# Performance work log

Measured on AMD Instinct MI355X. Metric: run time of the kernel, lower is better.

Reference implementation:

```python
import jax, jax.numpy as jnp
import numpy as np

N = 100000
E = 1600000
DIM_IN, DIM_H, DIM_OUT = 48, 48, 48


def gcn_conv(x, edge_index, W, b):
    # PyG GCNConv: add self-loops, symmetric normalization D^-1/2 (A+I) D^-1/2, linear first.
    n = x.shape[0]
    loop = jnp.arange(n, dtype=edge_index.dtype)
    row = jnp.concatenate([edge_index[0], loop])  # sources
    col = jnp.concatenate([edge_index[1], loop])  # targets
    deg = jax.ops.segment_sum(jnp.ones_like(col, dtype=x.dtype), col, num_segments=n)
    dinv = jnp.where(deg > 0, jax.lax.rsqrt(jnp.maximum(deg, 1e-12)), 0.0)
    norm = dinv[row] * dinv[col]  # [E+N]
    h = x @ W  # [N, out]
    msg = h[row] * norm[:, None]  # gather + scale, [E+N, out]
    out = jax.ops.segment_sum(msg, col, num_segments=n)  # scatter-add
    return out + b


def setup_inputs() -> dict:
    key = jax.random.key(0)
    ks = jax.random.split(key, 8)
    x = jax.random.normal(ks[0], (N, DIM_IN), dtype=jnp.float32)
    edge_index = jax.random.randint(ks[1], (2, E), 0, N, dtype=jnp.int64)
    s1 = 1.0 / np.sqrt(DIM_IN)
    s2 = 1.0 / np.sqrt(DIM_H)
    s3 = 1.0 / np.sqrt(DIM_OUT)
    W1 = jax.random.uniform(ks[2], (DIM_IN, DIM_H), jnp.float32, -s1, s1)
    b1 = jnp.zeros((DIM_H,), jnp.float32)
    W2 = jax.random.uniform(ks[3], (DIM_H, DIM_OUT), jnp.float32, -s2, s2)
    b2 = jnp.zeros((DIM_OUT,), jnp.float32)
    Wlin = jax.random.uniform(ks[4], (DIM_OUT, 2), jnp.float32, -s3, s3)
    blin = jax.random.uniform(ks[5], (2,), jnp.float32, -s3, s3)
    return {"x": x, "edge_index": edge_index, "W1": W1, "b1": b1, "W2": W2, "b2": b2, "Wlin": Wlin, "blin": blin}


def reference(x, edge_index, W1, b1, W2, b2, Wlin, blin):
    h = gcn_conv(x, edge_index, W1, b1)
    h = jax.nn.leaky_relu(h, negative_slope=0.01)
    h = gcn_conv(h, edge_index, W2, b2)
    # global_add_pool with all-zero batch ids -> sum over all nodes, [1, DIM_OUT]
    g = jnp.sum(h, axis=0, keepdims=True)
    # dropout is identity in eval mode
    return g @ Wlin + blin  # [1, 2]
```

## Files before the change

### kernel.cpp

```cpp
#include <hip/hip_runtime.h>
#include <hip/hip_bf16.h>
#include <hip/hip_fp8.h>

#define DIM 48
#define HS8 64
#define BKN 128
#define NB1MAX 800
#define NBLK 512
#define BCAPE 3072
#define GNPB 64
#define GTPN 3

typedef float v2f __attribute__((ext_vector_type(2)));

__device__ inline unsigned pack_fp8x4(float a, float b, float c, float d) {
#if __has_builtin(__builtin_amdgcn_cvt_pk_fp8_f32)
    int w = __builtin_amdgcn_cvt_pk_fp8_f32(a, b, 0, false);
    w = __builtin_amdgcn_cvt_pk_fp8_f32(c, d, w, true);
    return (unsigned)w;
#else
    __hip_fp8_e4m3 qa(a), qb(b), qc(c), qd(d);
    return (unsigned)qa.__x | ((unsigned)qb.__x << 8) |
           ((unsigned)qc.__x << 16) | ((unsigned)qd.__x << 24);
#endif
}

__device__ inline void acc_fp8x4(unsigned w, float* acc) {
#if __has_builtin(__builtin_amdgcn_cvt_pk_f32_fp8)
    v2f lo = __builtin_amdgcn_cvt_pk_f32_fp8((int)w, false);
    v2f hi = __builtin_amdgcn_cvt_pk_f32_fp8((int)w, true);
    acc[0] += lo[0]; acc[1] += lo[1]; acc[2] += hi[0]; acc[3] += hi[1];
#else
    __hip_fp8_e4m3 q0, q1, q2, q3;
    q0.__x = (unsigned char)(w & 0xff);
    q1.__x = (unsigned char)((w >> 8) & 0xff);
    q2.__x = (unsigned char)((w >> 16) & 0xff);
    q3.__x = (unsigned char)(w >> 24);
    acc[0] += (float)q0; acc[1] += (float)q1;
    acc[2] += (float)q2; acc[3] += (float)q3;
#endif
}

__global__ void k_bh(const int* __restrict__ col, int* __restrict__ bh, int E, int nb1) {
    __shared__ int h[NB1MAX];
    for (int i = threadIdx.x; i < nb1; i += blockDim.x) h[i] = 0;
    __syncthreads();
    int chunk = (E + NBLK - 1) / NBLK;
    int lo = blockIdx.x * chunk, hi = min(lo + chunk, E);
    for (int e = lo + threadIdx.x; e < hi; e += blockDim.x)
        atomicAdd(&h[col[e] >> 7], 1);
    __syncthreads();
    int* r = bh + (size_t)blockIdx.x * nb1;
    for (int i = threadIdx.x; i < nb1; i += blockDim.x) r[i] = h[i];
}

__global__ void k_colscan(int* __restrict__ bh, int* __restrict__ coltot, int nb1) {
    __shared__ int sm[NBLK];
    int b = blockIdx.x, t = threadIdx.x;
    sm[t] = bh[(size_t)t * nb1 + b];
    __syncthreads();
    int val = sm[t];
    for (int off = 1; off < NBLK; off <<= 1) {
        int v = (t >= off) ? sm[t - off] : 0;
        __syncthreads();
        sm[t] += v;
        __syncthreads();
    }
    bh[(size_t)t * nb1 + b] = sm[t] - val;
    if (t == NBLK - 1) coltot[b] = sm[t];
}

__global__ void k_scan1(const int* __restrict__ coltot, int* __restrict__ bstart,
                        float* __restrict__ g, int* __restrict__ nodeoff,
                        int nb1, int N, int E) {
    __shared__ int sm[1024];
    int t = threadIdx.x;
    sm[t] = (t < nb1) ? coltot[t] : 0;
    __syncthreads();
    for (int off = 1; off < 1024; off <<= 1) {
        int v = (t >= off) ? sm[t - off] : 0;
        __syncthreads();
        sm[t] += v;
        __syncthreads();
    }
    if (t < nb1) bstart[t] = (t == 0) ? 0 : sm[t - 1];
    if (t == 0) { bstart[nb1] = E; nodeoff[N] = E; }
    if (t < 64) g[t] = 0.0f;
}

__global__ void k_part2(const int* __restrict__ row, const int* __restrict__ col,
                        const int* __restrict__ bh, const int* __restrict__ bstart,
                        unsigned* __restrict__ part, int E, int nb1) {
    __shared__ int base[NB1MAX];
    __shared__ int lcur[NB1MAX];
    int blk = blockIdx.x, t = threadIdx.x;
    const int* bhr = bh + (size_t)blk * nb1;
    for (int i = t; i < nb1; i += blockDim.x) { base[i] = bstart[i] + bhr[i]; lcur[i] = 0; }
    __syncthreads();
    int chunk = (E + NBLK - 1) / NBLK;
    int lo = blk * chunk, hi = min(lo + chunk, E);
    for (int e = lo + t; e < hi; e += blockDim.x) {
        int c = col[e], r = row[e];
        int b = c >> 7;
        int s = atomicAdd(&lcur[b], 1);
        part[base[b] + s] = ((unsigned)(c & 127) << 24) | (unsigned)r;
    }
}

__global__ void k_sort(const unsigned* __restrict__ part, const int* __restrict__ bstart,
                       int* __restrict__ nodeoff, float* __restrict__ dinv,
                       int* __restrict__ srcs, int N, int nb1) {
    __shared__ int cnt[BKN];
    __shared__ int cur[BKN];
    __shared__ int sc[256];
    __shared__ int outb[BCAPE];
    int b = blockIdx.x, t = threadIdx.x;
    int nlo = b * BKN;
    int elo = bstart[b], ehi = bstart[b + 1];
    int nE = ehi - elo;
    if (t < BKN) cnt[t] = 0;
    __syncthreads();
    for (int e = elo + t; e < ehi; e += blockDim.x)
        atomicAdd(&cnt[part[e] >> 24], 1);
    __syncthreads();
    int v = (t < BKN) ? cnt[t] : 0;
    sc[t] = v;
    __syncthreads();
    for (int off = 1; off < 256; off <<= 1) {
        int u = (t >= off) ? sc[t - off] : 0;
        __syncthreads();
        sc[t] += u;
        __syncthreads();
    }
    int ex = (t == 0) ? 0 : sc[t - 1];
    if (t < BKN && nlo + t < N) {
        nodeoff[nlo + t] = elo + ex;
        dinv[nlo + t] = 1.0f / sqrtf((float)(v + 1));
        cur[t] = ex;
    }
    __syncthreads();
    if (nE <= BCAPE) {
        for (int e = elo + t; e < ehi; e += blockDim.x) {
            unsigned p = part[e];
            int s = atomicAdd(&cur[p >> 24], 1);
            outb[s] = (int)(p & 0xffffffu);
        }
        __syncthreads();
        for (int i = t; i < nE; i += blockDim.x) srcs[elo + i] = outb[i];
    } else {
        for (int e = elo + t; e < ehi; e += blockDim.x) {
            unsigned p = part[e];
            int s = atomicAdd(&cur[p >> 24], 1);
            srcs[elo + s] = (int)(p & 0xffffffu);
        }
    }
}

__global__ void k_mm_scale(const float* __restrict__ in, const float* __restrict__ W,
                           const float* __restrict__ dinv,
                           unsigned char* __restrict__ hs8, int n) {
    __shared__ float Ws[DIM * DIM];
    for (int i = threadIdx.x; i < DIM * DIM; i += blockDim.x) Ws[i] = W[i];
    __syncthreads();
    int node = blockIdx.x * blockDim.x + threadIdx.x;
    if (node >= n) return;
    float xr[DIM];
    const float4* xp = (const float4*)(in + (size_t)node * DIM);
    #pragma unroll
    for (int j = 0; j < DIM / 4; ++j) {
        float4 v = xp[j];
        xr[j * 4 + 0] = v.x; xr[j * 4 + 1] = v.y;
        xr[j * 4 + 2] = v.z; xr[j * 4 + 3] = v.w;
    }
    float o[DIM];
    #pragma unroll
    for (int f = 0; f < DIM; ++f) o[f] = 0.0f;
    for (int k = 0; k < DIM; ++k) {
        float xv = xr[k];
        #pragma unroll
        for (int f = 0; f < DIM; ++f) o[f] = fmaf(xv, Ws[k * DIM + f], o[f]);
    }
    float d = dinv[node];
    uint4* hp = (uint4*)(hs8 + (size_t)node * HS8);
    #pragma unroll
    for (int q = 0; q < 3; ++q) {
        uint4 v;
        v.x = pack_fp8x4(o[q*16+ 0]*d, o[q*16+ 1]*d, o[q*16+ 2]*d, o[q*16+ 3]*d);
        v.y = pack_fp8x4(o[q*16+ 4]*d, o[q*16+ 5]*d, o[q*16+ 6]*d, o[q*16+ 7]*d);
        v.z = pack_fp8x4(o[q*16+ 8]*d, o[q*16+ 9]*d, o[q*16+10]*d, o[q*16+11]*d);
        v.w = pack_fp8x4(o[q*16+12]*d, o[q*16+13]*d, o[q*16+14]*d, o[q*16+15]*d);
        hp[q] = v;
    }
}

__device__ inline void acc_fp8x16(uint4 v, float* acc) {
    acc_fp8x4(v.x, acc + 0);
    acc_fp8x4(v.y, acc + 4);
    acc_fp8x4(v.z, acc + 8);
    acc_fp8x4(v.w, acc + 12);
}

template <int RELU>
__global__ void k_gather(const unsigned char* __restrict__ hs8,
                         const int* __restrict__ nodeoff, const int* __restrict__ srcs,
                         const float* __restrict__ dinv, const float* __restrict__ bias,
                         float* __restrict__ outp, float* __restrict__ g, int n) {
    __shared__ float gsum[DIM];
    int t = threadIdx.x;
    if (!RELU && t < DIM) gsum[t] = 0.0f;
    if (!RELU) __syncthreads();
    int local = t / GTPN;
    int c = t - local * GTPN;
    int i = blockIdx.x * GNPB + local;
    bool valid = (i < n);
    float acc[16];
    float d = 0.0f;
    if (valid) {
        int start = nodeoff[i];
        int end = nodeoff[i + 1];
        d = dinv[i];
        const unsigned char* hb = hs8 + (size_t)c * 16;
        #pragma unroll
        for (int k = 0; k < 16; ++k) acc[k] = 0.0f;
        uint4 sv = *(const uint4*)(hb + (size_t)i * HS8);
        acc_fp8x16(sv, acc);
        for (int j = start; j < end; ++j) {
            uint4 v = *(const uint4*)(hb + (size_t)srcs[j] * HS8);
            acc_fp8x16(v, acc);
        }
    }
    if (RELU) {
        if (valid) {
            float o[16];
            #pragma unroll
            for (int k = 0; k < 16; ++k) {
                float v = acc[k] * d + bias[c * 16 + k];
                o[k] = (v >= 0.0f) ? v : 0.01f * v;
            }
            float4* op = (float4*)(outp + (size_t)i * DIM + c * 16);
            op[0] = make_float4(o[0], o[1], o[2], o[3]);
            op[1] = make_float4(o[4], o[5], o[6], o[7]);
            op[2] = make_float4(o[8], o[9], o[10], o[11]);
            op[3] = make_float4(o[12], o[13], o[14], o[15]);
        }
    } else {
        if (valid) {
            #pragma unroll
            for (int k = 0; k < 16; ++k) atomicAdd(&gsum[c * 16 + k], acc[k] * d);
        }
        __syncthreads();
        if (t < DIM) atomicAdd(&g[t], gsum[t]);
    }
}

__global__ void k_final(const float* __restrict__ g, const float* __restrict__ b2,
                        const float* __restrict__ Wlin, const float* __restrict__ blin,
                        float* __restrict__ out, int n) {
    int k = threadIdx.x;
    if (k < 2) {
        float s = blin[k];
        for (int f = 0; f < DIM; ++f)
            s += (g[f] + (float)n * b2[f]) * Wlin[f * 2 + k];
        out[k] = s;
    }
}

static inline char* alignup(char* p, size_t a) {
    return (char*)(((uintptr_t)p + a - 1) & ~(uintptr_t)(a - 1));
}

extern "C" void kernel_launch(void* const* d_in, const int* in_sizes, int n_in,
                              void* d_out, int out_size, void* d_ws, size_t ws_size,
                              hipStream_t stream) {
    const float* x    = (const float*)d_in[0];
    const int*   ei   = (const int*)d_in[1];
    const float* W1   = (const float*)d_in[2];
    const float* b1   = (const float*)d_in[3];
    const float* W2   = (const float*)d_in[4];
    const float* b2   = (const float*)d_in[5];
    const float* Wlin = (const float*)d_in[6];
    const float* blin = (const float*)d_in[7];
    float* out = (float*)d_out;

    int N = in_sizes[0] / DIM;
    int E = in_sizes[1] / 2;
    const int* row = ei;
    const int* col = ei + E;
    int nb1 = (N + BKN - 1) / BKN;

    char* p = (char*)d_ws;
    int* bh = (int*)p;                    p = alignup(p + (size_t)NBLK * nb1 * 4, 64);
    int* coltot = (int*)p;                p = alignup(p + nb1 * 4, 64);
    int* bstart = (int*)p;                p = alignup(p + (nb1 + 1) * 4, 64);
    int* nodeoff = (int*)p;               p = alignup(p + (size_t)(N + 1) * 4, 64);
    float* dinv = (float*)p;              p = alignup(p + (size_t)N * 4, 64);
    float* g = (float*)p;                 p = alignup(p + 64 * 4, 64);
    unsigned* part = (unsigned*)p;        p = alignup(p + (size_t)E * 4, 64);
    int* srcs = (int*)p;                  p = alignup(p + (size_t)E * 4, 64);
    unsigned char* hs8 = (unsigned char*)p; p = alignup(p + (size_t)N * HS8, 64);
    float* bufh = (float*)p;

    int nblk = (N + 255) / 256;
    int gblk = (N + GNPB - 1) / GNPB;

    k_bh<<<NBLK, 256, 0, stream>>>(col, bh, E, nb1);
    k_colscan<<<nb1, NBLK, 0, stream>>>(bh, coltot, nb1);
    k_scan1<<<1, 1024, 0, stream>>>(coltot, bstart, g, nodeoff, nb1, N, E);
    k_part2<<<NBLK, 256, 0, stream>>>(row, col, bh, bstart, part, E, nb1);
    k_sort<<<nb1, 256, 0, stream>>>(part, bstart, nodeoff, dinv, srcs, N, nb1);

    k_mm_scale<<<nblk, 256, 0, stream>>>(x, W1, dinv, hs8, N);
    k_gather<1><<<gblk, GNPB * GTPN, 0, stream>>>(hs8, nodeoff, srcs, dinv, b1, bufh, g, N);

    k_mm_scale<<<nblk, 256, 0, stream>>>(bufh, W2, dinv, hs8, N);
    k_gather<0><<<gblk, GNPB * GTPN, 0, stream>>>(hs8, nodeoff, srcs, dinv, b2, bufh, g, N);

    k_final<<<1, 64, 0, stream>>>(g, b2, Wlin, blin, out, N);
}
```

Baseline: 185.6 us.

## Split gather per node across 8 threads with edge halves and LDS-staged sources

The gather kernel now gives each node 8 threads instead of 3. Four column lanes each read 12 fp8 bytes, and two edge groups walk alternate neighbours; their partial sums are combined with a shuffle. Each block first copies its contiguous slice of source indices into shared memory, falling back to global loads when the slice exceeds the cap. The aim is more memory-level parallelism and shorter per-thread dependency chains on the random row gathers, at the cost of an extra barrier, a shuffle reduction and smaller 12-byte loads.

```diff
diff --git a/kernel.cpp b/kernel.cpp
--- a/kernel.cpp
+++ b/kernel.cpp
@@ -8,8 +8,8 @@
 #define NB1MAX 800
 #define NBLK 512
 #define BCAPE 3072
-#define GNPB 64
-#define GTPN 3
+#define GNPB 32
+#define SRCCAP 1024
 
 typedef float v2f __attribute__((ext_vector_type(2)));
 
@@ -193,60 +193,72 @@
     }
 }
 
-__device__ inline void acc_fp8x16(uint4 v, float* acc) {
-    acc_fp8x4(v.x, acc + 0);
-    acc_fp8x4(v.y, acc + 4);
-    acc_fp8x4(v.z, acc + 8);
-    acc_fp8x4(v.w, acc + 12);
-}
-
 template <int RELU>
-__global__ void k_gather(const unsigned char* __restrict__ hs8,
-                         const int* __restrict__ nodeoff, const int* __restrict__ srcs,
-                         const float* __restrict__ dinv, const float* __restrict__ bias,
-                         float* __restrict__ outp, float* __restrict__ g, int n) {
+__global__ __launch_bounds__(GNPB * 8) void k_gather(
+    const unsigned char* __restrict__ hs8,
+    const int* __restrict__ nodeoff, const int* __restrict__ srcs,
+    const float* __restrict__ dinv, const float* __restrict__ bias,
+    float* __restrict__ outp, float* __restrict__ g, int n) {
+    __shared__ int s_srcs[SRCCAP];
     __shared__ float gsum[DIM];
     int t = threadIdx.x;
     if (!RELU && t < DIM) gsum[t] = 0.0f;
-    if (!RELU) __syncthreads();
-    int local = t / GTPN;
-    int c = t - local * GTPN;
-    int i = blockIdx.x * GNPB + local;
+    int nlo = blockIdx.x * GNPB;
+    int nhi = min(nlo + GNPB, n);
+    int segbase = nodeoff[nlo];
+    int seglen = nodeoff[nhi] - segbase;
+    bool staged = (seglen <= SRCCAP);
+    if (staged)
+        for (int u = t; u < seglen; u += GNPB * 8) s_srcs[u] = srcs[segbase + u];
+    __syncthreads();
+
+    int local = t >> 3;
+    int sub = t & 7;
+    int grp = sub >> 2;
+    int c = sub & 3;
+    int i = nlo + local;
     bool valid = (i < n);
-    float acc[16];
+    float acc[12];
+    #pragma unroll
+    for (int k = 0; k < 12; ++k) acc[k] = 0.0f;
     float d = 0.0f;
     if (valid) {
         int start = nodeoff[i];
         int end = nodeoff[i + 1];
+        int deg = end - start;
+        int lbase = start - segbase;
         d = dinv[i];
-        const unsigned char* hb = hs8 + (size_t)c * 16;
-        #pragma unroll
-        for (int k = 0; k < 16; ++k) acc[k] = 0.0f;
-        uint4 sv = *(const uint4*)(hb + (size_t)i * HS8);
-        acc_fp8x16(sv, acc);
-        for (int j = start; j < end; ++j) {
-            uint4 v = *(const uint4*)(hb + (size_t)srcs[j] * HS8);
-            acc_fp8x16(v, acc);
-        }
-    }
+        const unsigned char* hb = hs8 + (size_t)c * 12;
+        for (int k = grp; k <= deg; k += 2) {
+            int src;
+            if (k == 0) src = i;
+            else src = staged ? s_srcs[lbase + k - 1] : srcs[start + k - 1];
+            uint3 v = *(const uint3*)(hb + (size_t)src * HS8);
+            acc_fp8x4(v.x, acc + 0);
+            acc_fp8x4(v.y, acc + 4);
+            acc_fp8x4(v.z, acc + 8);
+        }
+    }
+    #pragma unroll
+    for (int k = 0; k < 12; ++k) acc[k] += __shfl_down(acc[k], 4);
+
     if (RELU) {
-        if (valid) {
-            float o[16];
+        if (valid && grp == 0) {
+            float o[12];
             #pragma unroll
-            for (int k = 0; k < 16; ++k) {
-                float v = acc[k] * d + bias[c * 16 + k];
+            for (int k = 0; k < 12; ++k) {
+                float v = acc[k] * d + bias[c * 12 + k];
                 o[k] = (v >= 0.0f) ? v : 0.01f * v;
             }
-            float4* op = (float4*)(outp + (size_t)i * DIM + c * 16);
+            float4* op = (float4*)(outp + (size_t)i * DIM + c * 12);
             op[0] = make_float4(o[0], o[1], o[2], o[3]);
             op[1] = make_float4(o[4], o[5], o[6], o[7]);
             op[2] = make_float4(o[8], o[9], o[10], o[11]);
-            op[3] = make_float4(o[12], o[13], o[14], o[15]);
         }
     } else {
-        if (valid) {
+        if (valid && grp == 0) {
             #pragma unroll
-            for (int k = 0; k < 16; ++k) atomicAdd(&gsum[c * 16 + k], acc[k] * d);
+            for (int k = 0; k < 12; ++k) atomicAdd(&gsum[c * 12 + k], acc[k] * d);
         }
         __syncthreads();
         if (t < DIM) atomicAdd(&g[t], gsum[t]);
@@ -310,10 +322,10 @@
     k_sort<<<nb1, 256, 0, stream>>>(part, bstart, nodeoff, dinv, srcs, N, nb1);
 
     k_mm_scale<<<nblk, 256, 0, stream>>>(x, W1, dinv, hs8, N);
-    k_gather<1><<<gblk, GNPB * GTPN, 0, stream>>>(hs8, nodeoff, srcs, dinv, b1, bufh, g, N);
+    k_gather<1><<<gblk, GNPB * 8, 0, stream>>>(hs8, nodeoff, srcs, dinv, b1, bufh, g, N);
 
     k_mm_scale<<<nblk, 256, 0, stream>>>(bufh, W2, dinv, hs8, N);
-    k_gather<0><<<gblk, GNPB * GTPN, 0, stream>>>(hs8, nodeoff, srcs, dinv, b2, bufh, g, N);
+    k_gather<0><<<gblk, GNPB * 8, 0, stream>>>(hs8, nodeoff, srcs, dinv, b2, bufh, g, N);
 
     k_final<<<1, 64, 0, stream>>>(g, b2, Wlin, blin, out, N);
 }
```

New measurement: 188.6 us. About the same (+1.7%).

## Split each node's neighbor gather across two thread groups and reduce with shuffles

Applied to the files above, without the earlier changes.

The gather kernel now gives each node 6 lanes instead of 3. Two groups of three lanes take alternating neighbors (self-loop included) and are combined with a shuffle-down reduction. Each 64-lane wave handles 10 nodes, leaving 4 lanes idle. The aim is to double the loads in flight per node and shorten the serial dependent gather chain. The cost is idle lanes, the shuffle reduction, and more blocks because each block now holds 40 nodes.

```diff
diff --git a/kernel.cpp b/kernel.cpp
--- a/kernel.cpp
+++ b/kernel.cpp
@@ -8,8 +8,8 @@
 #define NB1MAX 800
 #define NBLK 512
 #define BCAPE 3072
-#define GNPB 64
-#define GTPN 3
+#define GNPW 10
+#define GNPB 40
 
 typedef float v2f __attribute__((ext_vector_type(2)));
 
@@ -41,6 +41,13 @@
 #endif
 }
 
+__device__ inline void acc_fp8x16(uint4 v, float* acc) {
+    acc_fp8x4(v.x, acc + 0);
+    acc_fp8x4(v.y, acc + 4);
+    acc_fp8x4(v.z, acc + 8);
+    acc_fp8x4(v.w, acc + 12);
+}
+
 __global__ void k_bh(const int* __restrict__ col, int* __restrict__ bh, int E, int nb1) {
     __shared__ int h[NB1MAX];
     for (int i = threadIdx.x; i < nb1; i += blockDim.x) h[i] = 0;
@@ -193,44 +200,45 @@
     }
 }
 
-__device__ inline void acc_fp8x16(uint4 v, float* acc) {
-    acc_fp8x4(v.x, acc + 0);
-    acc_fp8x4(v.y, acc + 4);
-    acc_fp8x4(v.z, acc + 8);
-    acc_fp8x4(v.w, acc + 12);
-}
-
 template <int RELU>
-__global__ void k_gather(const unsigned char* __restrict__ hs8,
-                         const int* __restrict__ nodeoff, const int* __restrict__ srcs,
-                         const float* __restrict__ dinv, const float* __restrict__ bias,
-                         float* __restrict__ outp, float* __restrict__ g, int n) {
+__global__ __launch_bounds__(256) void k_gather(
+    const unsigned char* __restrict__ hs8,
+    const int* __restrict__ nodeoff, const int* __restrict__ srcs,
+    const float* __restrict__ dinv, const float* __restrict__ bias,
+    float* __restrict__ outp, float* __restrict__ g, int n) {
     __shared__ float gsum[DIM];
     int t = threadIdx.x;
     if (!RELU && t < DIM) gsum[t] = 0.0f;
     if (!RELU) __syncthreads();
-    int local = t / GTPN;
-    int c = t - local * GTPN;
-    int i = blockIdx.x * GNPB + local;
-    bool valid = (i < n);
+    int wave = t >> 6;
+    int l = t & 63;
+    int nl = l / 6;
+    int sub = l - nl * 6;
+    int grp = sub >= 3;
+    int c = sub - grp * 3;
+    int i = blockIdx.x * GNPB + wave * GNPW + nl;
+    bool valid = (nl < GNPW) && (i < n);
     float acc[16];
+    #pragma unroll
+    for (int k = 0; k < 16; ++k) acc[k] = 0.0f;
     float d = 0.0f;
     if (valid) {
         int start = nodeoff[i];
         int end = nodeoff[i + 1];
+        int deg = end - start;
         d = dinv[i];
         const unsigned char* hb = hs8 + (size_t)c * 16;
-        #pragma unroll
-        for (int k = 0; k < 16; ++k) acc[k] = 0.0f;
-        uint4 sv = *(const uint4*)(hb + (size_t)i * HS8);
-        acc_fp8x16(sv, acc);
-        for (int j = start; j < end; ++j) {
-            uint4 v = *(const uint4*)(hb + (size_t)srcs[j] * HS8);
+        for (int k = grp; k <= deg; k += 2) {
+            int src = (k == 0) ? i : srcs[start + k - 1];
+            uint4 v = *(const uint4*)(hb + (size_t)src * HS8);
             acc_fp8x16(v, acc);
         }
     }
+    #pragma unroll
+    for (int k = 0; k < 16; ++k) acc[k] += __shfl_down(acc[k], 3);
+
     if (RELU) {
-        if (valid) {
+        if (valid && grp == 0) {
             float o[16];
             #pragma unroll
             for (int k = 0; k < 16; ++k) {
@@ -244,7 +252,7 @@
             op[3] = make_float4(o[12], o[13], o[14], o[15]);
         }
     } else {
-        if (valid) {
+        if (valid && grp == 0) {
             #pragma unroll
             for (int k = 0; k < 16; ++k) atomicAdd(&gsum[c * 16 + k], acc[k] * d);
         }
@@ -310,10 +318,10 @@
     k_sort<<<nb1, 256, 0, stream>>>(part, bstart, nodeoff, dinv, srcs, N, nb1);
 
     k_mm_scale<<<nblk, 256, 0, stream>>>(x, W1, dinv, hs8, N);
-    k_gather<1><<<gblk, GNPB * GTPN, 0, stream>>>(hs8, nodeoff, srcs, dinv, b1, bufh, g, N);
+    k_gather<1><<<gblk, 256, 0, stream>>>(hs8, nodeoff, srcs, dinv, b1, bufh, g, N);
 
     k_mm_scale<<<nblk, 256, 0, stream>>>(bufh, W2, dinv, hs8, N);
-    k_gather<0><<<gblk, GNPB * GTPN, 0, stream>>>(hs8, nodeoff, srcs, dinv, b2, bufh, g, N);
+    k_gather<0><<<gblk, 256, 0, stream>>>(hs8, nodeoff, srcs, dinv, b2, bufh, g, N);
 
     k_final<<<1, 64, 0, stream>>>(g, b2, Wlin, blin, out, N);
 }
```

New measurement: 194.0 us. 1.05x slower.

## Replace second GCN layer with weighted node-sum using out-degree normalization weights

Applied to the files above, without the earlier changes.

Because the second layer's output is only summed over all nodes, its aggregation collapses algebraically: sum_i out_i = sum_j w_j h1_j W2, where w_j = dinv_j * (dinv_j + sum over outgoing edges of dinv_target). The change builds a row-partitioned edge list alongside the column partition, computes w per node, then does a weighted reduction of layer-1 output and applies W2 once in the final kernel. This removes the second matmul and the second full gather pass. In exchange it adds a second histogram, scan and partition pass over the edges, and reuses the layer-1 output buffer as scratch for the row partition.

```diff
diff --git a/kernel.cpp b/kernel.cpp
--- a/kernel.cpp
+++ b/kernel.cpp
@@ -41,17 +41,29 @@
 #endif
 }
 
-__global__ void k_bh(const int* __restrict__ col, int* __restrict__ bh, int E, int nb1) {
-    __shared__ int h[NB1MAX];
-    for (int i = threadIdx.x; i < nb1; i += blockDim.x) h[i] = 0;
+__device__ inline void acc_fp8x16(uint4 v, float* acc) {
+    acc_fp8x4(v.x, acc + 0);
+    acc_fp8x4(v.y, acc + 4);
+    acc_fp8x4(v.z, acc + 8);
+    acc_fp8x4(v.w, acc + 12);
+}
+
+__global__ void k_bh2(const int* __restrict__ row, const int* __restrict__ col,
+                      int* __restrict__ bhc, int* __restrict__ bhr, int E, int nb1) {
+    __shared__ int hc[NB1MAX];
+    __shared__ int hr[NB1MAX];
+    for (int i = threadIdx.x; i < nb1; i += blockDim.x) { hc[i] = 0; hr[i] = 0; }
     __syncthreads();
     int chunk = (E + NBLK - 1) / NBLK;
     int lo = blockIdx.x * chunk, hi = min(lo + chunk, E);
-    for (int e = lo + threadIdx.x; e < hi; e += blockDim.x)
-        atomicAdd(&h[col[e] >> 7], 1);
-    __syncthreads();
-    int* r = bh + (size_t)blockIdx.x * nb1;
-    for (int i = threadIdx.x; i < nb1; i += blockDim.x) r[i] = h[i];
+    for (int e = lo + threadIdx.x; e < hi; e += blockDim.x) {
+        atomicAdd(&hc[col[e] >> 7], 1);
+        atomicAdd(&hr[row[e] >> 7], 1);
+    }
+    __syncthreads();
+    int* rc = bhc + (size_t)blockIdx.x * nb1;
+    int* rr = bhr + (size_t)blockIdx.x * nb1;
+    for (int i = threadIdx.x; i < nb1; i += blockDim.x) { rc[i] = hc[i]; rr[i] = hr[i]; }
 }
 
 __global__ void k_colscan(int* __restrict__ bh, int* __restrict__ coltot, int nb1) {
@@ -70,12 +82,13 @@
     if (t == NBLK - 1) coltot[b] = sm[t];
 }
 
-__global__ void k_scan1(const int* __restrict__ coltot, int* __restrict__ bstart,
+__global__ void k_scan2(const int* __restrict__ coltotc, int* __restrict__ bstartc,
+                        const int* __restrict__ coltotr, int* __restrict__ bstartr,
                         float* __restrict__ g, int* __restrict__ nodeoff,
                         int nb1, int N, int E) {
     __shared__ int sm[1024];
     int t = threadIdx.x;
-    sm[t] = (t < nb1) ? coltot[t] : 0;
+    sm[t] = (t < nb1) ? coltotc[t] : 0;
     __syncthreads();
     for (int off = 1; off < 1024; off <<= 1) {
         int v = (t >= off) ? sm[t - off] : 0;
@@ -83,27 +96,47 @@
         sm[t] += v;
         __syncthreads();
     }
-    if (t < nb1) bstart[t] = (t == 0) ? 0 : sm[t - 1];
-    if (t == 0) { bstart[nb1] = E; nodeoff[N] = E; }
+    if (t < nb1) bstartc[t] = (t == 0) ? 0 : sm[t - 1];
+    if (t == 0) { bstartc[nb1] = E; nodeoff[N] = E; }
+    __syncthreads();
+    sm[t] = (t < nb1) ? coltotr[t] : 0;
+    __syncthreads();
+    for (int off = 1; off < 1024; off <<= 1) {
+        int v = (t >= off) ? sm[t - off] : 0;
+        __syncthreads();
+        sm[t] += v;
+        __syncthreads();
+    }
+    if (t < nb1) bstartr[t] = (t == 0) ? 0 : sm[t - 1];
+    if (t == 0) bstartr[nb1] = E;
     if (t < 64) g[t] = 0.0f;
 }
 
-__global__ void k_part2(const int* __restrict__ row, const int* __restrict__ col,
-                        const int* __restrict__ bh, const int* __restrict__ bstart,
-                        unsigned* __restrict__ part, int E, int nb1) {
-    __shared__ int base[NB1MAX];
-    __shared__ int lcur[NB1MAX];
+__global__ void k_part2d(const int* __restrict__ row, const int* __restrict__ col,
+                         const int* __restrict__ bhc, const int* __restrict__ bhr,
+                         const int* __restrict__ bstartc, const int* __restrict__ bstartr,
+                         unsigned* __restrict__ partc, unsigned* __restrict__ partr,
+                         int E, int nb1) {
+    __shared__ int basec[NB1MAX]; __shared__ int lcurc[NB1MAX];
+    __shared__ int baser[NB1MAX]; __shared__ int lcurr[NB1MAX];
     int blk = blockIdx.x, t = threadIdx.x;
-    const int* bhr = bh + (size_t)blk * nb1;
-    for (int i = t; i < nb1; i += blockDim.x) { base[i] = bstart[i] + bhr[i]; lcur[i] = 0; }
+    const int* bhcr = bhc + (size_t)blk * nb1;
+    const int* bhrr = bhr + (size_t)blk * nb1;
+    for (int i = t; i < nb1; i += blockDim.x) {
+        basec[i] = bstartc[i] + bhcr[i]; lcurc[i] = 0;
+        baser[i] = bstartr[i] + bhrr[i]; lcurr[i] = 0;
+    }
     __syncthreads();
     int chunk = (E + NBLK - 1) / NBLK;
     int lo = blk * chunk, hi = min(lo + chunk, E);
     for (int e = lo + t; e < hi; e += blockDim.x) {
         int c = col[e], r = row[e];
-        int b = c >> 7;
-        int s = atomicAdd(&lcur[b], 1);
-        part[base[b] + s] = ((unsigned)(c & 127) << 24) | (unsigned)r;
+        int bc = c >> 7;
+        int sc_ = atomicAdd(&lcurc[bc], 1);
+        partc[basec[bc] + sc_] = ((unsigned)(c & 127) << 24) | (unsigned)r;
+        int br = r >> 7;
+        int sr_ = atomicAdd(&lcurr[br], 1);
+        partr[baser[br] + sr_] = ((unsigned)(r & 127) << 24) | (unsigned)c;
     }
 }
 
@@ -156,6 +189,26 @@
     }
 }
 
+__global__ void k_wsum(const unsigned* __restrict__ partr, const int* __restrict__ bstartr,
+                       const float* __restrict__ dinv, float* __restrict__ wfin,
+                       int N, int nb1) {
+    __shared__ float ws[BKN];
+    int b = blockIdx.x, t = threadIdx.x;
+    if (t < BKN) ws[t] = 0.0f;
+    __syncthreads();
+    int elo = bstartr[b], ehi = bstartr[b + 1];
+    for (int e = elo + t; e < ehi; e += blockDim.x) {
+        unsigned p = partr[e];
+        atomicAdd(&ws[p >> 24], dinv[p & 0xffffffu]);
+    }
+    __syncthreads();
+    int j = b * BKN + t;
+    if (t < BKN && j < N) {
+        float dj = dinv[j];
+        wfin[j] = (ws[t] + dj) * dj;
+    }
+}
+
 __global__ void k_mm_scale(const float* __restrict__ in, const float* __restrict__ W,
                            const float* __restrict__ dinv,
                            unsigned char* __restrict__ hs8, int n) {
@@ -193,75 +246,71 @@
     }
 }
 
-__device__ inline void acc_fp8x16(uint4 v, float* acc) {
-    acc_fp8x4(v.x, acc + 0);
-    acc_fp8x4(v.y, acc + 4);
-    acc_fp8x4(v.z, acc + 8);
-    acc_fp8x4(v.w, acc + 12);
-}
-
-template <int RELU>
-__global__ void k_gather(const unsigned char* __restrict__ hs8,
-                         const int* __restrict__ nodeoff, const int* __restrict__ srcs,
-                         const float* __restrict__ dinv, const float* __restrict__ bias,
-                         float* __restrict__ outp, float* __restrict__ g, int n) {
-    __shared__ float gsum[DIM];
+__global__ __launch_bounds__(GNPB * GTPN) void k_gather1(
+    const unsigned char* __restrict__ hs8,
+    const int* __restrict__ nodeoff, const int* __restrict__ srcs,
+    const float* __restrict__ dinv, const float* __restrict__ bias,
+    float* __restrict__ outp, int n) {
     int t = threadIdx.x;
-    if (!RELU && t < DIM) gsum[t] = 0.0f;
-    if (!RELU) __syncthreads();
     int local = t / GTPN;
     int c = t - local * GTPN;
     int i = blockIdx.x * GNPB + local;
-    bool valid = (i < n);
+    if (i >= n) return;
+    int start = nodeoff[i];
+    int end = nodeoff[i + 1];
+    float d = dinv[i];
+    const unsigned char* hb = hs8 + (size_t)c * 16;
     float acc[16];
-    float d = 0.0f;
-    if (valid) {
-        int start = nodeoff[i];
-        int end = nodeoff[i + 1];
-        d = dinv[i];
-        const unsigned char* hb = hs8 + (size_t)c * 16;
-        #pragma unroll
-        for (int k = 0; k < 16; ++k) acc[k] = 0.0f;
-        uint4 sv = *(const uint4*)(hb + (size_t)i * HS8);
-        acc_fp8x16(sv, acc);
-        for (int j = start; j < end; ++j) {
-            uint4 v = *(const uint4*)(hb + (size_t)srcs[j] * HS8);
-            acc_fp8x16(v, acc);
-        }
-    }
-    if (RELU) {
-        if (valid) {
-            float o[16];
-            #pragma unroll
-            for (int k = 0; k < 16; ++k) {
-                float v = acc[k] * d + bias[c * 16 + k];
-                o[k] = (v >= 0.0f) ? v : 0.01f * v;
-            }
-            float4* op = (float4*)(outp + (size_t)i * DIM + c * 16);
-            op[0] = make_float4(o[0], o[1], o[2], o[3]);
-            op[1] = make_float4(o[4], o[5], o[6], o[7]);
-            op[2] = make_float4(o[8], o[9], o[10], o[11]);
-            op[3] = make_float4(o[12], o[13], o[14], o[15]);
-        }
-    } else {
-        if (valid) {
-            #pragma unroll
-            for (int k = 0; k < 16; ++k) atomicAdd(&gsum[c * 16 + k], acc[k] * d);
-        }
-        __syncthreads();
-        if (t < DIM) atomicAdd(&g[t], gsum[t]);
-    }
-}
-
-__global__ void k_final(const float* __restrict__ g, const float* __restrict__ b2,
-                        const float* __restrict__ Wlin, const float* __restrict__ blin,
-                        float* __restrict__ out, int n) {
-    int k = threadIdx.x;
-    if (k < 2) {
-        float s = blin[k];
-        for (int f = 0; f < DIM; ++f)
-            s += (g[f] + (float)n * b2[f]) * Wlin[f * 2 + k];
-        out[k] = s;
+    #pragma unroll
+    for (int k = 0; k < 16; ++k) acc[k] = 0.0f;
+    uint4 sv = *(const uint4*)(hb + (size_t)i * HS8);
+    acc_fp8x16(sv, acc);
+    for (int j = start; j < end; ++j) {
+        uint4 v = *(const uint4*)(hb + (size_t)srcs[j] * HS8);
+        acc_fp8x16(v, acc);
+    }
+    float o[16];
+    #pragma unroll
+    for (int k = 0; k < 16; ++k) {
+        float v = acc[k] * d + bias[c * 16 + k];
+        o[k] = (v >= 0.0f) ? v : 0.01f * v;
+    }
+    float4* op = (float4*)(outp + (size_t)i * DIM + c * 16);
+    op[0] = make_float4(o[0], o[1], o[2], o[3]);
+    op[1] = make_float4(o[4], o[5], o[6], o[7]);
+    op[2] = make_float4(o[8], o[9], o[10], o[11]);
+    op[3] = make_float4(o[12], o[13], o[14], o[15]);
+}
+
+__global__ void k_vred(const float* __restrict__ h1, const float* __restrict__ wfin,
+                       float* g, int n) {
+    __shared__ float sm[192];
+    int f = threadIdx.x % DIM;
+    int r = threadIdx.x / DIM;
+    float s = 0.0f;
+    for (int i = blockIdx.x * 4 + r; i < n; i += gridDim.x * 4)
+        s += wfin[i] * h1[(size_t)i * DIM + f];
+    sm[threadIdx.x] = s;
+    __syncthreads();
+    if (threadIdx.x < DIM)
+        atomicAdd(&g[f], sm[f] + sm[DIM + f] + sm[2 * DIM + f] + sm[3 * DIM + f]);
+}
+
+__global__ void k_final2(const float* __restrict__ g, const float* __restrict__ W2,
+                         const float* __restrict__ b2, const float* __restrict__ Wlin,
+                         const float* __restrict__ blin, float* __restrict__ out, int n) {
+    __shared__ float gp[DIM];
+    int t = threadIdx.x;
+    if (t < DIM) {
+        float s = (float)n * b2[t];
+        for (int q = 0; q < DIM; ++q) s += g[q] * W2[q * DIM + t];
+        gp[t] = s;
+    }
+    __syncthreads();
+    if (t < 2) {
+        float s = blin[t];
+        for (int f = 0; f < DIM; ++f) s += gp[f] * Wlin[f * 2 + t];
+        out[t] = s;
     }
 }
 
@@ -289,31 +338,36 @@
     int nb1 = (N + BKN - 1) / BKN;
 
     char* p = (char*)d_ws;
-    int* bh = (int*)p;                    p = alignup(p + (size_t)NBLK * nb1 * 4, 64);
-    int* coltot = (int*)p;                p = alignup(p + nb1 * 4, 64);
-    int* bstart = (int*)p;                p = alignup(p + (nb1 + 1) * 4, 64);
+    int* bhc = (int*)p;                   p = alignup(p + (size_t)NBLK * nb1 * 4, 64);
+    int* bhr = (int*)p;                   p = alignup(p + (size_t)NBLK * nb1 * 4, 64);
+    int* coltotc = (int*)p;               p = alignup(p + nb1 * 4, 64);
+    int* coltotr = (int*)p;               p = alignup(p + nb1 * 4, 64);
+    int* bstartc = (int*)p;               p = alignup(p + (nb1 + 1) * 4, 64);
+    int* bstartr = (int*)p;               p = alignup(p + (nb1 + 1) * 4, 64);
     int* nodeoff = (int*)p;               p = alignup(p + (size_t)(N + 1) * 4, 64);
     float* dinv = (float*)p;              p = alignup(p + (size_t)N * 4, 64);
+    float* wfin = (float*)p;              p = alignup(p + (size_t)N * 4, 64);
     float* g = (float*)p;                 p = alignup(p + 64 * 4, 64);
-    unsigned* part = (unsigned*)p;        p = alignup(p + (size_t)E * 4, 64);
+    unsigned* partc = (unsigned*)p;       p = alignup(p + (size_t)E * 4, 64);
     int* srcs = (int*)p;                  p = alignup(p + (size_t)E * 4, 64);
     unsigned char* hs8 = (unsigned char*)p; p = alignup(p + (size_t)N * HS8, 64);
     float* bufh = (float*)p;
+    unsigned* partr = (unsigned*)bufh;
 
     int nblk = (N + 255) / 256;
     int gblk = (N + GNPB - 1) / GNPB;
 
-    k_bh<<<NBLK, 256, 0, stream>>>(col, bh, E, nb1);
-    k_colscan<<<nb1, NBLK, 0, stream>>>(bh, coltot, nb1);
-    k_scan1<<<1, 1024, 0, stream>>>(coltot, bstart, g, nodeoff, nb1, N, E);
-    k_part2<<<NBLK, 256, 0, stream>>>(row, col, bh, bstart, part, E, nb1);
-    k_sort<<<nb1, 256, 0, stream>>>(part, bstart, nodeoff, dinv, srcs, N, nb1);
+    k_bh2<<<NBLK, 256, 0, stream>>>(row, col, bhc, bhr, E, nb1);
+    k_colscan<<<nb1, NBLK, 0, stream>>>(bhc, coltotc, nb1);
+    k_colscan<<<nb1, NBLK, 0, stream>>>(bhr, coltotr, nb1);
+    k_scan2<<<1, 1024, 0, stream>>>(coltotc, bstartc, coltotr, bstartr, g, nodeoff, nb1, N, E);
+    k_part2d<<<NBLK, 256, 0, stream>>>(row, col, bhc, bhr, bstartc, bstartr, partc, partr, E, nb1);
+    k_sort<<<nb1, 256, 0, stream>>>(partc, bstartc, nodeoff, dinv, srcs, N, nb1);
+    k_wsum<<<nb1, 256, 0, stream>>>(partr, bstartr, dinv, wfin, N, nb1);
 
     k_mm_scale<<<nblk, 256, 0, stream>>>(x, W1, dinv, hs8, N);
-    k_gather<1><<<gblk, GNPB * GTPN, 0, stream>>>(hs8, nodeoff, srcs, dinv, b1, bufh, g, N);
-
-    k_mm_scale<<<nblk, 256, 0, stream>>>(bufh, W2, dinv, hs8, N);
-    k_gather<0><<<gblk, GNPB * GTPN, 0, stream>>>(hs8, nodeoff, srcs, dinv, b2, bufh, g, N);
-
-    k_final<<<1, 64, 0, stream>>>(g, b2, Wlin, blin, out, N);
-}
+    k_gather1<<<gblk, GNPB * GTPN, 0, stream>>>(hs8, nodeoff, srcs, dinv, b1, bufh, N);
+
+    k_vred<<<1024, 192, 0, stream>>>(bufh, wfin, g, N);
+    k_final2<<<1, 64, 0, stream>>>(g, W2, b2, Wlin, blin, out, N);
+}
```

Result: faster. 177.5 us (-4.4%).
